# Kernel tuning notes

Hardware: AMD Instinct MI355X
Metric: run time of the kernel (lower is better)

## Reference

```python
import jax, jax.numpy as jnp
import numpy as np

N = 8192        # num nodes == input_dim (attn is [N,N], indexed by edge endpoints)
E = 262144      # num edges (nnz of sparse G), avg degree 32
OD = 64         # output_dim


def setup_inputs() -> dict:
    key = jax.random.key(0)
    k_x, k_r, k_c, k_v, k_a, k_w = jax.random.split(key, 6)
    x = jax.random.normal(k_x, (N, N), dtype=jnp.float32)
    row = jax.random.randint(k_r, (E,), 0, N)
    col = jax.random.randint(k_c, (E,), 0, N)
    values = jax.random.uniform(k_v, (E,), dtype=jnp.float32)
    attn = jax.random.uniform(k_a, (N, N), dtype=jnp.float32)  # init uniform(0,1) per reset_parameters
    stdv = 1.0 / np.sqrt(OD)
    weight = jax.random.uniform(k_w, (N, OD), dtype=jnp.float32, minval=-stdv, maxval=stdv)
    return {"x": x, "attn": attn, "weight": weight, "values": values, "row": row, "col": col}


def reference(x, attn, weight, values, row, col):
    # x = x @ W : [N, OD]
    y = x @ weight
    # sparse_dense_mul: scale each edge's value by attn[row, col] (irregular gather)
    ev = values * attn[row, col]                      # [E]
    # torch.sparse.mm(G, y): out[i] = sum_{e: row[e]==i} ev[e] * y[col[e]]
    out = jax.ops.segment_sum(ev[:, None] * y[col], row, num_segments=x.shape[0])
    return (out, jnp.linalg.norm(attn))
```

## Files before the change

kernel.cpp:

```cpp
#include <hip/hip_runtime.h>
#include <hip/hip_bf16.h>

#define N 8192
#define OD 64
#define E_EDGES 262144

#define BM 64
#define KSPLIT 16
#define KS_PER_SPLIT (N / KSPLIT)
#define SCAT_BLOCKS 8192
#define EDGE_ITERS (E_EDGES / (SCAT_BLOCKS * 4))

typedef __attribute__((ext_vector_type(8))) short bf16x8;
typedef __attribute__((ext_vector_type(4))) float f32x4;

__device__ __forceinline__ unsigned short f2bf(float f) {
    union { float f; unsigned u; } v; v.f = f;
    unsigned r = (v.u + 0x7fffu + ((v.u >> 16) & 1u)) >> 16;
    return (unsigned short)r;
}

__device__ __forceinline__ unsigned pack_trunc(unsigned lo, unsigned hi) {
#if defined(__has_builtin) && __has_builtin(__builtin_amdgcn_perm)
    return __builtin_amdgcn_perm(hi, lo, 0x07060302u);
#else
    return (lo >> 16) | (hi & 0xFFFF0000u);
#endif
}

__device__ __forceinline__ void gload16(const void* g, void* l) {
    __builtin_amdgcn_global_load_lds(
        (const __attribute__((address_space(1))) unsigned int*)g,
        (__attribute__((address_space(3))) unsigned int*)l, 16, 0, 0);
}

__global__ __launch_bounds__(256) void prep_kernel(const float* __restrict__ w,
                                                   unsigned short* __restrict__ wt,
                                                   float4* __restrict__ y4,
                                                   float4* __restrict__ out4) {
    const int bid = blockIdx.x, t = threadIdx.x;
    const int base = bid * 256 + t;
    float4 z{0.f, 0.f, 0.f, 0.f};
    #pragma unroll
    for (int u = 0; u < 4; ++u) y4[base + u * 32768] = z;
    #pragma unroll
    for (int u = 0; u < 4; ++u) out4[base + u * 32768] = z;

    __shared__ unsigned short lds[64][80];
    const int kb = bid * 64;
    #pragma unroll
    for (int p = 0; p < 4; ++p) {
        int idx = p * 1024 + t * 4;
        int r = idx >> 6, c = idx & 63;
        float4 v = *(const float4*)(&w[(size_t)(kb + r) * OD + c]);
        lds[c + 0][r] = f2bf(v.x);
        lds[c + 1][r] = f2bf(v.y);
        lds[c + 2][r] = f2bf(v.z);
        lds[c + 3][r] = f2bf(v.w);
    }
    __syncthreads();
    const int colx = t >> 2, j0 = (t & 3) * 16;
    #pragma unroll
    for (int u = 0; u < 2; ++u) {
        *(bf16x8*)(wt + (size_t)colx * N + kb + j0 + u * 8) =
            *(const bf16x8*)(&lds[colx][j0 + u * 8]);
    }
}

__global__ __launch_bounds__(256) void gemm_kernel(const float* __restrict__ x,
                                                   const unsigned short* __restrict__ wt,
                                                   float* __restrict__ y) {
    __shared__ unsigned short blds[64 * 512];

    const int t = threadIdx.x;
    const int wv = t >> 6, lane = t & 63;
    const int lrow = lane & 15, g = lane >> 4;
    const int row = blockIdx.x * BM + wv * 16 + lrow;
    const int k0 = blockIdx.y * KS_PER_SPLIT;
    const int bkey = (lrow & 7) << 3;

    #pragma unroll
    for (int j = 0; j < 16; ++j) {
        const int brow = j * 4 + wv;
        gload16(wt + (size_t)brow * N + k0 + ((lane ^ (brow & 7)) << 3),
                &blds[brow * 512 + lane * 8]);
    }
    asm volatile("s_waitcnt vmcnt(0)" ::: "memory");
    __builtin_amdgcn_sched_barrier(0);
    __builtin_amdgcn_s_barrier();

    f32x4 acc[4] = {f32x4{0,0,0,0}, f32x4{0,0,0,0}, f32x4{0,0,0,0}, f32x4{0,0,0,0}};
    const float* xp = x + (size_t)row * N + k0 + g * 8;
    uint4 xb[8];
    bf16x8 A[4];

    #define LOADQ(q)                                                  \
        _Pragma("unroll")                                             \
        for (int i = 0; i < 4; ++i) {                                 \
            xb[2*i]   = *(const uint4*)(xp + (q) * 128 + i * 32);     \
            xb[2*i+1] = *(const uint4*)(xp + (q) * 128 + i * 32 + 4); \
        }

    #define PACKQ()                                                   \
        _Pragma("unroll")                                             \
        for (int i = 0; i < 4; ++i) {                                 \
            union { bf16x8 v; unsigned u[4]; } Au;                    \
            Au.u[0] = pack_trunc(xb[2*i].x,   xb[2*i].y);             \
            Au.u[1] = pack_trunc(xb[2*i].z,   xb[2*i].w);             \
            Au.u[2] = pack_trunc(xb[2*i+1].x, xb[2*i+1].y);           \
            Au.u[3] = pack_trunc(xb[2*i+1].z, xb[2*i+1].w);           \
            A[i] = Au.v;                                              \
        }

    #define MFMAQ(q)                                                              \
        _Pragma("unroll")                                                         \
        for (int ks = 0; ks < 4; ++ks) {                                          \
            _Pragma("unroll")                                                     \
            for (int cf = 0; cf < 4; ++cf) {                                      \
                bf16x8 b = *(const bf16x8*)&blds[(cf * 16 + lrow) * 512 +         \
                                (((q) * 128 + ks * 32 + g * 8) ^ bkey)];          \
                acc[cf] = __builtin_amdgcn_mfma_f32_16x16x32_bf16(A[ks], b,       \
                                                                  acc[cf], 0,0,0);\
            }                                                                     \
        }

    LOADQ(0);
    PACKQ(); LOADQ(1); MFMAQ(0);
    PACKQ(); LOADQ(2); MFMAQ(1);
    PACKQ(); LOADQ(3); MFMAQ(2);
    PACKQ();           MFMAQ(3);

    float* yp = y + ((size_t)blockIdx.x * BM + wv * 16 + g * 4) * OD;
    #pragma unroll
    for (int cf = 0; cf < 4; ++cf) {
        #pragma unroll
        for (int i = 0; i < 4; ++i)
            atomicAdd(&yp[i * OD + cf * 16 + lrow], acc[cf][i]);
    }
    #undef LOADQ
    #undef PACKQ
    #undef MFMAQ
}

__device__ __forceinline__ void do_scatter(const float* __restrict__ values,
                                           const float* __restrict__ attn,
                                           const int* __restrict__ row,
                                           const int* __restrict__ col,
                                           const float* __restrict__ y,
                                           float* __restrict__ out,
                                           int bid, int t) {
    const int lane = t & 63;
    const int w = t >> 6;
    int r8[EDGE_ITERS], c8[EDGE_ITERS];
    float v8[EDGE_ITERS], a8[EDGE_ITERS];
    #pragma unroll
    for (int i = 0; i < EDGE_ITERS; ++i) {
        int e = bid * 4 + w + i * (SCAT_BLOCKS * 4);
        r8[i] = row[e]; c8[i] = col[e]; v8[i] = values[e];
    }
    #pragma unroll
    for (int i = 0; i < EDGE_ITERS; ++i)
        a8[i] = attn[(size_t)r8[i] * N + c8[i]];
    #pragma unroll
    for (int i = 0; i < EDGE_ITERS; ++i) {
        float yv = y[c8[i] * OD + lane];
        atomicAdd(&out[r8[i] * OD + lane], v8[i] * a8[i] * yv);
    }
}

__device__ __forceinline__ float do_norm_part(const float* __restrict__ attn, int bid, int t) {
    const float4* a4 = (const float4*)attn;
    float s = 0.f;
    int i = bid * 256 + t;
    #pragma unroll
    for (int u = 0; u < 8; ++u) {
        float4 v = a4[i + u * (SCAT_BLOCKS * 256)];
        s += v.x * v.x + v.y * v.y + v.z * v.z + v.w * v.w;
    }
    return s;
}

__global__ __launch_bounds__(256) void scatter_norm_kernel(
        const float* __restrict__ values, const float* __restrict__ attn,
        const int* __restrict__ row, const int* __restrict__ col,
        const float* __restrict__ y, float* __restrict__ out,
        float* __restrict__ part) {
    const int bid = blockIdx.x, t = threadIdx.x;
    float s;
    if (bid & 1) {
        s = do_norm_part(attn, bid, t);
        do_scatter(values, attn, row, col, y, out, bid, t);
    } else {
        do_scatter(values, attn, row, col, y, out, bid, t);
        s = do_norm_part(attn, bid, t);
    }
    for (int off = 32; off > 0; off >>= 1) s += __shfl_down(s, off, 64);
    __shared__ float wpart[4];
    int wid = t >> 6;
    if ((t & 63) == 0) wpart[wid] = s;
    __syncthreads();
    if (t == 0) part[bid] = wpart[0] + wpart[1] + wpart[2] + wpart[3];
}

__global__ __launch_bounds__(256) void finalize_kernel(const float* __restrict__ part,
                                                       float* __restrict__ out_norm) {
    float s = 0.f;
    #pragma unroll
    for (int k = 0; k < SCAT_BLOCKS / 256; ++k) s += part[k * 256 + threadIdx.x];
    for (int off = 32; off > 0; off >>= 1) s += __shfl_down(s, off, 64);
    __shared__ float wp[4];
    int wid = threadIdx.x >> 6;
    if ((threadIdx.x & 63) == 0) wp[wid] = s;
    __syncthreads();
    if (threadIdx.x == 0) *out_norm = sqrtf(wp[0] + wp[1] + wp[2] + wp[3]);
}

extern "C" void kernel_launch(void* const* d_in, const int* in_sizes, int n_in,
                              void* d_out, int out_size, void* d_ws, size_t ws_size,
                              hipStream_t stream) {
    const float* x      = (const float*)d_in[0];
    const float* attn   = (const float*)d_in[1];
    const float* weight = (const float*)d_in[2];
    const float* values = (const float*)d_in[3];
    const int*   row    = (const int*)d_in[4];
    const int*   col    = (const int*)d_in[5];
    float* out = (float*)d_out;

    char* wsb = (char*)d_ws;
    float*          part = (float*)wsb;
    unsigned short* wt   = (unsigned short*)(wsb + (1u << 20));
    float*          y    = (float*)(wsb + (2u << 20));

    prep_kernel<<<128, 256, 0, stream>>>(weight, wt, (float4*)y, (float4*)out);
    gemm_kernel<<<dim3(N / BM, KSPLIT), 256, 0, stream>>>(x, wt, y);
    scatter_norm_kernel<<<SCAT_BLOCKS, 256, 0, stream>>>(values, attn, row, col, y, out, part);
    finalize_kernel<<<1, 256, 0, stream>>>(part, out + (size_t)N * OD);
}
```

Before: 165.9 us.

## Replace split-K GEMM with full-K row tiles and double-buffered B staging

```diff
diff --git a/kernel.cpp b/kernel.cpp
--- a/kernel.cpp
+++ b/kernel.cpp
@@ -5,9 +5,9 @@
 #define OD 64
 #define E_EDGES 262144
 
-#define BM 64
-#define KSPLIT 16
-#define KS_PER_SPLIT (N / KSPLIT)
+#define GBM 16
+#define GCHUNK 256
+#define NCHUNK (N / GCHUNK)
 #define SCAT_BLOCKS 8192
 #define EDGE_ITERS (E_EDGES / (SCAT_BLOCKS * 4))
 
@@ -70,76 +70,85 @@
 __global__ __launch_bounds__(256) void gemm_kernel(const float* __restrict__ x,
                                                    const unsigned short* __restrict__ wt,
                                                    float* __restrict__ y) {
-    __shared__ unsigned short blds[64 * 512];
+    __shared__ unsigned short blds[2][64 * GCHUNK];
 
     const int t = threadIdx.x;
     const int wv = t >> 6, lane = t & 63;
     const int lrow = lane & 15, g = lane >> 4;
-    const int row = blockIdx.x * BM + wv * 16 + lrow;
-    const int k0 = blockIdx.y * KS_PER_SPLIT;
-    const int bkey = (lrow & 7) << 3;
-
-    #pragma unroll
-    for (int j = 0; j < 16; ++j) {
-        const int brow = j * 4 + wv;
-        gload16(wt + (size_t)brow * N + k0 + ((lane ^ (brow & 7)) << 3),
-                &blds[brow * 512 + lane * 8]);
-    }
+    const int r0 = blockIdx.x * GBM;
+    const int row = r0 + lrow;
+    const int brow = wv * 16 + lrow;
+    const int key = (lrow & 7) << 3;
+
+    #define STAGE_B(buf, c)                                                        \
+        {                                                                          \
+            const int kc = (c) * GCHUNK;                                           \
+            _Pragma("unroll")                                                      \
+            for (int j = 0; j < 8; ++j) {                                          \
+                int idx = j * 256 + t;                                \
+                int br = idx >> 5;                                 \
+                int ch = idx & 31;                        \
+                gload16(wt + (size_t)br * N + kc + ((ch ^ (br & 7)) << 3),         \
+                        &blds[buf][idx * 8]);                                      \
+            }                                                                      \
+        }
+
+    f32x4 acc = f32x4{0.f, 0.f, 0.f, 0.f};
+    const float* xp = x + (size_t)row * N + g * 8;
+    uint4 xb[8];
+    bf16x8 A[4];
+
+    #define LOADH(c, h)                                                            \
+        _Pragma("unroll")                                                          \
+        for (int i = 0; i < 4; ++i) {                                              \
+            xb[2*i]   = *(const uint4*)(xp + (c) * GCHUNK + (h) * 128 + i * 32);   \
+            xb[2*i+1] = *(const uint4*)(xp + (c) * GCHUNK + (h) * 128 + i * 32 + 4);\
+        }
+
+    #define PACKH()                                                                \
+        _Pragma("unroll")                                                          \
+        for (int i = 0; i < 4; ++i) {                                              \
+            union { bf16x8 v; unsigned u[4]; } Au;                                 \
+            Au.u[0] = pack_trunc(xb[2*i].x,   xb[2*i].y);                          \
+            Au.u[1] = pack_trunc(xb[2*i].z,   xb[2*i].w);                          \
+            Au.u[2] = pack_trunc(xb[2*i+1].x, xb[2*i+1].y);                        \
+            Au.u[3] = pack_trunc(xb[2*i+1].z, xb[2*i+1].w);                        \
+            A[i] = Au.v;                                                           \
+        }
+
+    #define MFMAH(buf, h)                                                          \
+        _Pragma("unroll")                                                          \
+        for (int i = 0; i < 4; ++i) {                                              \
+            const int ko = ((h) * 4 + i) * 32 + g * 8;                             \
+            bf16x8 b = *(const bf16x8*)&blds[buf][brow * GCHUNK + (ko ^ key)];     \
+            acc = __builtin_amdgcn_mfma_f32_16x16x32_bf16(A[i], b, acc, 0, 0, 0); \
+        }
+
+    STAGE_B(0, 0);
     asm volatile("s_waitcnt vmcnt(0)" ::: "memory");
     __builtin_amdgcn_sched_barrier(0);
     __builtin_amdgcn_s_barrier();
 
-    f32x4 acc[4] = {f32x4{0,0,0,0}, f32x4{0,0,0,0}, f32x4{0,0,0,0}, f32x4{0,0,0,0}};
-    const float* xp = x + (size_t)row * N + k0 + g * 8;
-    uint4 xb[8];
-    bf16x8 A[4];
-
-    #define LOADQ(q)                                                  \
-        _Pragma("unroll")                                             \
-        for (int i = 0; i < 4; ++i) {                                 \
-            xb[2*i]   = *(const uint4*)(xp + (q) * 128 + i * 32);     \
-            xb[2*i+1] = *(const uint4*)(xp + (q) * 128 + i * 32 + 4); \
-        }
-
-    #define PACKQ()                                                   \
-        _Pragma("unroll")                                             \
-        for (int i = 0; i < 4; ++i) {                                 \
-            union { bf16x8 v; unsigned u[4]; } Au;                    \
-            Au.u[0] = pack_trunc(xb[2*i].x,   xb[2*i].y);             \
-            Au.u[1] = pack_trunc(xb[2*i].z,   xb[2*i].w);             \
-            Au.u[2] = pack_trunc(xb[2*i+1].x, xb[2*i+1].y);           \
-            Au.u[3] = pack_trunc(xb[2*i+1].z, xb[2*i+1].w);           \
-            A[i] = Au.v;                                              \
-        }
-
-    #define MFMAQ(q)                                                              \
-        _Pragma("unroll")                                                         \
-        for (int ks = 0; ks < 4; ++ks) {                                          \
-            _Pragma("unroll")                                                     \
-            for (int cf = 0; cf < 4; ++cf) {                                      \
-                bf16x8 b = *(const bf16x8*)&blds[(cf * 16 + lrow) * 512 +         \
-                                (((q) * 128 + ks * 32 + g * 8) ^ bkey)];          \
-                acc[cf] = __builtin_amdgcn_mfma_f32_16x16x32_bf16(A[ks], b,       \
-                                                                  acc[cf], 0,0,0);\
-            }                                                                     \
-        }
-
-    LOADQ(0);
-    PACKQ(); LOADQ(1); MFMAQ(0);
-    PACKQ(); LOADQ(2); MFMAQ(1);
-    PACKQ(); LOADQ(3); MFMAQ(2);
-    PACKQ();           MFMAQ(3);
-
-    float* yp = y + ((size_t)blockIdx.x * BM + wv * 16 + g * 4) * OD;
-    #pragma unroll
-    for (int cf = 0; cf < 4; ++cf) {
-        #pragma unroll
-        for (int i = 0; i < 4; ++i)
-            atomicAdd(&yp[i * OD + cf * 16 + lrow], acc[cf][i]);
-    }
-    #undef LOADQ
-    #undef PACKQ
-    #undef MFMAQ
+    for (int c = 0; c < NCHUNK; ++c) {
+        const int buf = c & 1;
+        if (c + 1 < NCHUNK) STAGE_B(buf ^ 1, c + 1);
+        __builtin_amdgcn_sched_barrier(0);
+        LOADH(c, 0);
+        PACKH(); LOADH(c, 1); MFMAH(buf, 0);
+        PACKH();              MFMAH(buf, 1);
+        asm volatile("s_waitcnt vmcnt(0)" ::: "memory");
+        __builtin_amdgcn_sched_barrier(0);
+        __builtin_amdgcn_s_barrier();
+    }
+
+    #pragma unroll
+    for (int i = 0; i < 4; ++i)
+        y[(size_t)(r0 + g * 4 + i) * OD + wv * 16 + lrow] = acc[i];
+
+    #undef STAGE_B
+    #undef LOADH
+    #undef PACKH
+    #undef MFMAH
 }
 
 __device__ __forceinline__ void do_scatter(const float* __restrict__ values,
@@ -232,7 +241,7 @@
     float*          y    = (float*)(wsb + (2u << 20));
 
     prep_kernel<<<128, 256, 0, stream>>>(weight, wt, (float4*)y, (float4*)out);
-    gemm_kernel<<<dim3(N / BM, KSPLIT), 256, 0, stream>>>(x, wt, y);
+    gemm_kernel<<<N / GBM, 256, 0, stream>>>(x, wt, y);
     scatter_norm_kernel<<<SCAT_BLOCKS, 256, 0, stream>>>(values, attn, row, col, y, out, part);
     finalize_kernel<<<1, 256, 0, stream>>>(part, out + (size_t)N * OD);
 }
```

Result: slower. 245.2 us (+47.8%).
